# Kernel tuning notes

Measured on AMD Instinct MI355X. Metric: run time of the kernel, lower is better.

Reference implementation:

```python
import jax, jax.numpy as jnp
import numpy as np

B, S, D = 32, 8192, 128
SPARSITY = 0.5
CLUSTER = 4
HID = 256
MEM = 128
NCLS = 10
MASK_KEY = jax.random.key(1234)


def setup_inputs() -> dict:
    key = jax.random.key(0)
    ks = jax.random.split(key, 8)
    cin = CLUSTER * D  # 512
    return {
        "x": jax.random.normal(ks[0], (B, S, D), dtype=jnp.float32),
        "memory": jax.random.normal(ks[1], (B, MEM), dtype=jnp.float32),
        "W_fc": jax.random.normal(ks[2], (HID, cin), dtype=jnp.float32) / np.sqrt(cin),
        "b_fc": jax.random.normal(ks[3], (HID,), dtype=jnp.float32) * 0.01,
        "W_mem": jax.random.normal(ks[4], (MEM, HID), dtype=jnp.float32) / np.sqrt(HID),
        "b_mem": jax.random.normal(ks[5], (MEM,), dtype=jnp.float32) * 0.01,
        "W_out": jax.random.normal(ks[6], (NCLS, MEM), dtype=jnp.float32) / np.sqrt(MEM),
        "b_out": jax.random.normal(ks[7], (NCLS,), dtype=jnp.float32) * 0.01,
    }


def reference(x, memory, W_fc, b_fc, W_mem, b_mem, W_out, b_out):
    # --- SparseInformationExtraction: top-k tokens by L2 norm ---
    k = int(SPARSITY * S)  # 4096
    token_norms = jnp.linalg.norm(x, axis=-1)          # (B, S)
    _, topk_idx = jax.lax.top_k(token_norms, k)        # (B, k), sorted desc like torch.topk
    sparse_x = jnp.take_along_axis(x, topk_idx[:, :, None], axis=1)  # (B, k, D)

    # --- HierarchicalClustering: group CLUSTER tokens ---
    num_clusters = k // CLUSTER                        # 1024
    clustered = sparse_x.reshape(B, num_clusters, CLUSTER * D)  # (B, 1024, 512)

    # --- DynamicMaskingActivation: linear + bernoulli mask + relu ---
    h = jnp.einsum('bnc,hc->bnh', clustered, W_fc) + b_fc       # (B, 1024, HID)
    mask = jax.random.bernoulli(MASK_KEY, p=SPARSITY, shape=h.shape).astype(h.dtype)
    h = jax.nn.relu(h * mask)

    # --- SparseMemory: mean-pool + linear + residual relu ---
    x_compressed = jnp.mean(h, axis=1)                           # (B, HID)
    updated_memory = jax.nn.relu(x_compressed @ W_mem.T + b_mem + memory)  # (B, MEM)

    # --- output head ---
    output = updated_memory @ W_out.T + b_out                    # (B, NCLS)
    return (output, updated_memory)
```

## Files before the change

### kernel.cpp

```cpp
#include <hip/hip_runtime.h>
#include <stdint.h>

#define NB 32
#define NS 8192
#define ND 128
#define KTOP 4096
#define NCLUST 1024
#define CIN 512
#define HIDN 256
#define NMEM 128
#define NCLS 10
#define HALFCNT 4194304u

typedef unsigned long long ull;
typedef __attribute__((ext_vector_type(8))) short bf16x8;
typedef __attribute__((ext_vector_type(4))) float f32x4;

__device__ __forceinline__ unsigned int rotl32(unsigned int v, int r) {
  return (v << r) | (v >> (32 - r));
}

__device__ __forceinline__ void threefry_block(unsigned int& x0, unsigned int& x1) {
  const unsigned int k0 = 0u;
  const unsigned int k1 = 1234u;
  const unsigned int k2 = 0x1BD11BDAu ^ 0u ^ 1234u;
  x0 += k0; x1 += k1;
#define TF_R(r) { x0 += x1; x1 = rotl32(x1, (r)); x1 ^= x0; }
  TF_R(13) TF_R(15) TF_R(26) TF_R(6)   x0 += k1; x1 += k2 + 1u;
  TF_R(17) TF_R(29) TF_R(16) TF_R(24)  x0 += k2; x1 += k0 + 2u;
  TF_R(13) TF_R(15) TF_R(26) TF_R(6)   x0 += k0; x1 += k1 + 3u;
  TF_R(17) TF_R(29) TF_R(16) TF_R(24)  x0 += k1; x1 += k2 + 4u;
  TF_R(13) TF_R(15) TF_R(26) TF_R(6)   x0 += k2; x1 += k0 + 5u;
#undef TF_R
}

__device__ __forceinline__ bool mask_keep(unsigned int flat) {
  const bool low = flat < HALFCNT;
  unsigned int a, b;
  if (low) { a = flat;           b = flat + HALFCNT; }
  else     { a = flat - HALFCNT; b = flat; }
  threefry_block(a, b);
  const unsigned int w = low ? a : b;
  return (w & 0x80000000u) == 0u;
}

__device__ __forceinline__ unsigned int f2bf(float f) {
  unsigned int u = __float_as_uint(f);
  return (u + 0x7fffu + ((u >> 16) & 1u)) >> 16;
}
__device__ __forceinline__ unsigned int pack2bf(float lo, float hi) {
  return f2bf(lo) | (f2bf(hi) << 16);
}

__device__ __forceinline__ void gload_lds16(const void* g, void* l) {
  __builtin_amdgcn_global_load_lds(
      (const __attribute__((address_space(1))) unsigned int*)g,
      (__attribute__((address_space(3))) unsigned int*)l, 16, 0, 0);
}

__device__ __forceinline__ ull shfl_xor_u64(ull x, int m) {
  unsigned int lo = (unsigned int)x, hi = (unsigned int)(x >> 32);
  lo = (unsigned int)__shfl_xor((int)lo, m);
  hi = (unsigned int)__shfl_xor((int)hi, m);
  return ((ull)hi << 32) | lo;
}

__global__ __launch_bounds__(256) void wprep_kernel(
    const float* __restrict__ Wfc, unsigned short* __restrict__ Wbf) {
  const int t = blockIdx.x * 256 + threadIdx.x;
  const float4* s = (const float4*)(Wfc + (size_t)t * 8);
  const float4 a = s[0], b = s[1];
  uint4 o;
  o.x = pack2bf(a.x, a.y); o.y = pack2bf(a.z, a.w);
  o.z = pack2bf(b.x, b.y); o.w = pack2bf(b.z, b.w);
  *(uint4*)(Wbf + (size_t)t * 8) = o;
}

__global__ __launch_bounds__(256) void norms_kernel(
    const float* __restrict__ x, ull* __restrict__ keys,
    float* __restrict__ xc) {
  const int t = blockIdx.x * 256 + threadIdx.x;
  if (t < NB * HIDN) xc[t] = 0.0f;
  const int token = t >> 5;
  const int l = t & 31;
  const float4 v = ((const float4*)(x + (size_t)token * ND))[l];
  float ss = v.x * v.x + v.y * v.y + v.z * v.z + v.w * v.w;
#pragma unroll
  for (int off = 16; off >= 1; off >>= 1) ss += __shfl_xor(ss, off);
  if (l == 0) {
    const float nrm = sqrtf(ss);
    const unsigned int ub = ~__float_as_uint(nrm);
    keys[token] = ((ull)ub << 32) | (unsigned int)(token & (NS - 1));
  }
}

#define CMPEX(J)                                                        \
  {                                                                     \
    _Pragma("unroll") for (int r = 0; r < 8; ++r) {                     \
      if ((r & (J)) == 0) {                                             \
        const int i0 = (tid << 3) + r;                                  \
        const bool up2 = ((i0 & k) == 0);                               \
        const ull lo = v[r], hi = v[r | (J)];                           \
        const ull mn = lo < hi ? lo : hi;                               \
        const ull mx = lo < hi ? hi : lo;                               \
        v[r] = up2 ? mn : mx;                                           \
        v[r | (J)] = up2 ? mx : mn;                                     \
      }                                                                 \
    }                                                                   \
  }

__global__ __launch_bounds__(1024) void sort_kernel(
    const ull* __restrict__ keys, unsigned int* __restrict__ topk) {
  __shared__ ull slds[NS];
  const int b = blockIdx.x;
  const int tid = threadIdx.x;
  ull v[8];
  const ull* src = keys + (size_t)b * NS + tid * 8;
#pragma unroll
  for (int r = 0; r < 8; ++r) v[r] = src[r];

  for (int k = 2; k <= NS; k <<= 1) {
    for (int j = k >> 1; j >= 512; j >>= 1) {
      __syncthreads();
#pragma unroll
      for (int r = 0; r < 8; ++r) slds[r * 1024 + tid] = v[r];
      __syncthreads();
      const int ptid = tid ^ (j >> 3);
      const bool up2 = (((tid << 3) & k) == 0);
      const bool lower = (((tid << 3) & j) == 0);
      const bool keepmin = (up2 == lower);
#pragma unroll
      for (int r = 0; r < 8; ++r) {
        const ull p = slds[r * 1024 + ptid];
        const ull mn = v[r] < p ? v[r] : p;
        const ull mx = v[r] < p ? p : v[r];
        v[r] = keepmin ? mn : mx;
      }
    }
    {
      int jstart = (k >> 1) < 256 ? (k >> 1) : 256;
      for (int j = jstart; j >= 8; j >>= 1) {
        const int lanemask = j >> 3;
        const bool up2 = (((tid << 3) & k) == 0);
        const bool lower = (((tid << 3) & j) == 0);
        const bool keepmin = (up2 == lower);
#pragma unroll
        for (int r = 0; r < 8; ++r) {
          const ull p = shfl_xor_u64(v[r], lanemask);
          const ull mn = v[r] < p ? v[r] : p;
          const ull mx = v[r] < p ? p : v[r];
          v[r] = keepmin ? mn : mx;
        }
      }
    }
    if (k >= 8)      { CMPEX(4) CMPEX(2) CMPEX(1) }
    else if (k == 4) { CMPEX(2) CMPEX(1) }
    else             { CMPEX(1) }
  }

  if (tid < KTOP / 8) {
#pragma unroll
    for (int r = 0; r < 8; ++r)
      topk[b * KTOP + tid * 8 + r] = (unsigned int)v[r];
  }
}

__global__ __launch_bounds__(256) void gemm_kernel(
    const float* __restrict__ x, const unsigned short* __restrict__ Wbf,
    const float* __restrict__ bfc, const unsigned int* __restrict__ topk,
    float* __restrict__ xc) {
  __shared__ __align__(16) unsigned short Al[128 * 64];
  __shared__ __align__(16) unsigned short Bl[128 * 64];
  __shared__ int tokL[512];
  __shared__ float red[4][64];

  const int bid = blockIdx.x;
  const int m0 = bid * 128;
  const int bb = bid >> 3;
  const int n0 = blockIdx.y * 128;
  const int t = threadIdx.x;
  const int w = t >> 6, l = t & 63;
  const int wr = w >> 1, wc = w & 1;
  const int lrow = l & 15, lk = l >> 4;

  {
    const int base = bb * KTOP + (bid & 7) * 512;
    tokL[t] = (int)topk[base + t];
    tokL[t + 256] = (int)topk[base + t + 256];
  }
  __syncthreads();

  f32x4 acc[4][4];
#pragma unroll
  for (int m = 0; m < 4; ++m)
#pragma unroll
    for (int n = 0; n < 4; ++n) acc[m][n] = (f32x4)0.f;

  const int arow = t >> 1, kh = t & 1;
  float4 ar[8];
  {
    const int token = tokL[arow * 4 + 0];
    const float* asrc = x + ((size_t)bb * NS + token) * ND + kh * 32;
#pragma unroll
    for (int q = 0; q < 8; ++q) ar[q] = ((const float4*)asrc)[q];
  }

  const int brow_in8 = l >> 3;
  const int bkb_src = ((l & 7) * 16) ^ (brow_in8 << 4);

  for (int kt = 0; kt < 8; ++kt) {
    {
      const int kb0 = kh * 64;
#pragma unroll
      for (int c = 0; c < 4; ++c) {
        const float4 lo = ar[c * 2], hi = ar[c * 2 + 1];
        uint4 pw;
        pw.x = pack2bf(lo.x, lo.y); pw.y = pack2bf(lo.z, lo.w);
        pw.z = pack2bf(hi.x, hi.y); pw.w = pack2bf(hi.z, hi.w);
        const int kb = kb0 + c * 16;
        const int off = arow * 128 + (kb ^ ((arow & 7) << 4));
        *(uint4*)((char*)Al + off) = pw;
      }
    }
    {
#pragma unroll
      for (int q = 0; q < 4; ++q) {
        const int grp = w * 4 + q;
        const int row = grp * 8 + brow_in8;
        const char* g = (const char*)Wbf + (size_t)(n0 + row) * 1024 +
                        kt * 128 + bkb_src;
        gload_lds16(g, (char*)Bl + grp * 1024);
      }
    }
    __syncthreads();

    if (kt < 7) {
      const int c = kt + 1;
      const int token = tokL[arow * 4 + (c >> 1)];
      const float* asrc =
          x + ((size_t)bb * NS + token) * ND + (c & 1) * 64 + kh * 32;
#pragma unroll
      for (int q = 0; q < 8; ++q) ar[q] = ((const float4*)asrc)[q];
    }

    const int swz = (lrow & 7) << 4;
#pragma unroll
    for (int kk = 0; kk < 2; ++kk) {
      const int koff = (kk * 64 + lk * 16) ^ swz;
      bf16x8 af[4], bfr[4];
#pragma unroll
      for (int m = 0; m < 4; ++m)
        af[m] = *(const bf16x8*)((const char*)Al +
                                 (wr * 64 + m * 16 + lrow) * 128 + koff);
#pragma unroll
      for (int n = 0; n < 4; ++n)
        bfr[n] = *(const bf16x8*)((const char*)Bl +
                                  (wc * 64 + n * 16 + lrow) * 128 + koff);
#pragma unroll
      for (int m = 0; m < 4; ++m)
#pragma unroll
        for (int n = 0; n < 4; ++n)
          acc[m][n] = __builtin_amdgcn_mfma_f32_16x16x32_bf16(
              af[m], bfr[n], acc[m][n], 0, 0, 0);
    }
    __syncthreads();
  }

  float bias_n[4];
#pragma unroll
  for (int n = 0; n < 4; ++n) bias_n[n] = bfc[n0 + wc * 64 + n * 16 + lrow];

  const int rowbase = m0 + wr * 64 + lk * 4;
  float csum[4] = {0.f, 0.f, 0.f, 0.f};
#pragma unroll
  for (int n = 0; n < 4; ++n) {
    const unsigned int gcol = (unsigned int)(n0 + wc * 64 + n * 16 + lrow);
#pragma unroll
    for (int m = 0; m < 4; ++m) {
#pragma unroll
      for (int reg = 0; reg < 4; ++reg) {
        const unsigned int gm = (unsigned int)(rowbase + m * 16 + reg);
        const unsigned int flat = gm * 256u + gcol;
        const bool keep = mask_keep(flat);
        float vv = acc[m][n][reg] + bias_n[n];
        vv = keep ? fmaxf(vv, 0.0f) : 0.0f;
        csum[n] += vv;
      }
    }
  }
#pragma unroll
  for (int n = 0; n < 4; ++n) {
    csum[n] += __shfl_xor(csum[n], 16);
    csum[n] += __shfl_xor(csum[n], 32);
  }
  if (l < 16) {
#pragma unroll
    for (int n = 0; n < 4; ++n) red[w][n * 16 + l] = csum[n];
  }
  __syncthreads();
  if (t < 128) {
    const int cwc = t >> 6, c = t & 63;
    const float s = red[cwc][c] + red[cwc + 2][c];
    atomicAdd(&xc[bb * HIDN + n0 + t], s);
  }
}

__global__ __launch_bounds__(128) void tail_kernel(
    const float* __restrict__ xc, const float* __restrict__ memory,
    const float* __restrict__ Wmem, const float* __restrict__ bmem,
    const float* __restrict__ Wout, const float* __restrict__ bout,
    float* __restrict__ out) {
  __shared__ __align__(16) float xl[HIDN];
  __shared__ float ul[NMEM];
  const int b = blockIdx.x, t = threadIdx.x;
  xl[t]       = xc[b * HIDN + t] * (1.0f / NCLUST);
  xl[t + 128] = xc[b * HIDN + t + 128] * (1.0f / NCLUST);
  __syncthreads();
  float a = 0.0f;
  const float4* wr2 = (const float4*)(Wmem + (size_t)t * HIDN);
#pragma unroll 4
  for (int q = 0; q < HIDN / 4; ++q) {
    const float4 wv = wr2[q];
    const float4 xv = *(const float4*)&xl[q * 4];
    a = fmaf(wv.x, xv.x, a); a = fmaf(wv.y, xv.y, a);
    a = fmaf(wv.z, xv.z, a); a = fmaf(wv.w, xv.w, a);
  }
  a += bmem[t] + memory[b * NMEM + t];
  a = fmaxf(a, 0.0f);
  ul[t] = a;
  out[NB * NCLS + b * NMEM + t] = a;
  __syncthreads();
  if (t < NCLS) {
    float o = 0.0f;
#pragma unroll 4
    for (int m = 0; m < NMEM; ++m) o = fmaf(ul[m], Wout[t * NMEM + m], o);
    out[b * NCLS + t] = o + bout[t];
  }
}

extern "C" void kernel_launch(void* const* d_in, const int* in_sizes, int n_in,
                              void* d_out, int out_size, void* d_ws, size_t ws_size,
                              hipStream_t stream) {
  (void)in_sizes; (void)n_in; (void)out_size; (void)ws_size;
  const float* x    = (const float*)d_in[0];
  const float* mem  = (const float*)d_in[1];
  const float* Wfc  = (const float*)d_in[2];
  const float* bfc  = (const float*)d_in[3];
  const float* Wmem = (const float*)d_in[4];
  const float* bmem = (const float*)d_in[5];
  const float* Wout = (const float*)d_in[6];
  const float* bout = (const float*)d_in[7];
  float* out = (float*)d_out;

  char* ws = (char*)d_ws;
  ull* keys = (ull*)ws;
  unsigned int* topk = (unsigned int*)(ws + (size_t)NB * NS * 8);
  float* xc = (float*)(ws + (size_t)NB * NS * 8 + (size_t)NB * KTOP * 4);
  unsigned short* Wbf = (unsigned short*)(ws + (size_t)NB * NS * 8 +
                                          (size_t)NB * KTOP * 4 +
                                          (size_t)NB * HIDN * 4);

  wprep_kernel<<<dim3(HIDN * CIN / (256 * 8)), 256, 0, stream>>>(Wfc, Wbf);
  norms_kernel<<<dim3(NB * NS / 8), 256, 0, stream>>>(x, keys, xc);
  sort_kernel<<<dim3(NB), 1024, 0, stream>>>(keys, topk);
  gemm_kernel<<<dim3(256, 2), 256, 0, stream>>>(x, Wbf, bfc, topk, xc);
  tail_kernel<<<dim3(NB), 128, 0, stream>>>(xc, mem, Wmem, bmem, Wout, bout, out);
}
```

Measured before the change: 305.5 us.

## Split bitonic sort across two blocks per batch, widen GEMM tile, fuse weight prep

The per-batch 8192-key bitonic sort is split in two. A first kernel sorts each 4096-key half in opposite directions on 64 blocks. A second kernel takes the elementwise min of the two halves, which gives a bitonic sequence holding the top 4096, and runs only the final half-merge. The GEMM now covers all 256 hidden columns per 512-thread block, so each gathered x row is loaded once instead of twice. The weight bf16 conversion is folded into extra blocks of the norms kernel to save a launch. The cost is more sort launches and a bigger LDS footprint in the GEMM.

```diff
diff --git a/kernel.cpp b/kernel.cpp
--- a/kernel.cpp
+++ b/kernel.cpp
@@ -65,21 +65,23 @@
   return ((ull)hi << 32) | lo;
 }
 
-__global__ __launch_bounds__(256) void wprep_kernel(
-    const float* __restrict__ Wfc, unsigned short* __restrict__ Wbf) {
-  const int t = blockIdx.x * 256 + threadIdx.x;
-  const float4* s = (const float4*)(Wfc + (size_t)t * 8);
-  const float4 a = s[0], b = s[1];
-  uint4 o;
-  o.x = pack2bf(a.x, a.y); o.y = pack2bf(a.z, a.w);
-  o.z = pack2bf(b.x, b.y); o.w = pack2bf(b.z, b.w);
-  *(uint4*)(Wbf + (size_t)t * 8) = o;
-}
-
+#define NORM_BLOCKS 32768
 __global__ __launch_bounds__(256) void norms_kernel(
     const float* __restrict__ x, ull* __restrict__ keys,
-    float* __restrict__ xc) {
-  const int t = blockIdx.x * 256 + threadIdx.x;
+    float* __restrict__ xc, const float* __restrict__ Wfc,
+    unsigned short* __restrict__ Wbf) {
+  const int blk = blockIdx.x;
+  if (blk >= NORM_BLOCKS) {
+    const int t = (blk - NORM_BLOCKS) * 256 + threadIdx.x;
+    const float4* s = (const float4*)(Wfc + (size_t)t * 8);
+    const float4 a = s[0], b = s[1];
+    uint4 o;
+    o.x = pack2bf(a.x, a.y); o.y = pack2bf(a.z, a.w);
+    o.z = pack2bf(b.x, b.y); o.w = pack2bf(b.z, b.w);
+    *(uint4*)(Wbf + (size_t)t * 8) = o;
+    return;
+  }
+  const int t = blk * 256 + threadIdx.x;
   if (t < NB * HIDN) xc[t] = 0.0f;
   const int token = t >> 5;
   const int l = t & 31;
@@ -94,12 +96,12 @@
   }
 }
 
-#define CMPEX(J)                                                        \
+#define CMPEX(J, K, HF)                                                 \
   {                                                                     \
     _Pragma("unroll") for (int r = 0; r < 8; ++r) {                     \
       if ((r & (J)) == 0) {                                             \
         const int i0 = (tid << 3) + r;                                  \
-        const bool up2 = ((i0 & k) == 0);                               \
+        const bool up2 = (((i0 & (K)) == 0) != (HF));                   \
         const ull lo = v[r], hi = v[r | (J)];                           \
         const ull mn = lo < hi ? lo : hi;                               \
         const ull mx = lo < hi ? hi : lo;                               \
@@ -109,39 +111,40 @@
     }                                                                   \
   }
 
-__global__ __launch_bounds__(1024) void sort_kernel(
-    const ull* __restrict__ keys, unsigned int* __restrict__ topk) {
-  __shared__ ull slds[NS];
-  const int b = blockIdx.x;
+__global__ __launch_bounds__(512) void sortA_kernel(ull* __restrict__ keys) {
+  __shared__ ull slds[8 * 512];
+  const int b = blockIdx.x >> 1;
+  const int half = blockIdx.x & 1;
+  const bool hf = (half != 0);
   const int tid = threadIdx.x;
   ull v[8];
-  const ull* src = keys + (size_t)b * NS + tid * 8;
-#pragma unroll
-  for (int r = 0; r < 8; ++r) v[r] = src[r];
-
-  for (int k = 2; k <= NS; k <<= 1) {
+  ull* base = keys + (size_t)b * NS + half * 4096;
+#pragma unroll
+  for (int r = 0; r < 8; ++r) v[r] = base[tid * 8 + r];
+
+  for (int k = 2; k <= 4096; k <<= 1) {
     for (int j = k >> 1; j >= 512; j >>= 1) {
       __syncthreads();
 #pragma unroll
-      for (int r = 0; r < 8; ++r) slds[r * 1024 + tid] = v[r];
+      for (int r = 0; r < 8; ++r) slds[r * 512 + tid] = v[r];
       __syncthreads();
       const int ptid = tid ^ (j >> 3);
-      const bool up2 = (((tid << 3) & k) == 0);
+      const bool up2 = ((((tid << 3) & k) == 0) != hf);
       const bool lower = (((tid << 3) & j) == 0);
       const bool keepmin = (up2 == lower);
 #pragma unroll
       for (int r = 0; r < 8; ++r) {
-        const ull p = slds[r * 1024 + ptid];
+        const ull p = slds[r * 512 + ptid];
         const ull mn = v[r] < p ? v[r] : p;
         const ull mx = v[r] < p ? p : v[r];
         v[r] = keepmin ? mn : mx;
       }
     }
     {
-      int jstart = (k >> 1) < 256 ? (k >> 1) : 256;
+      const int jstart = (k >> 1) < 256 ? (k >> 1) : 256;
       for (int j = jstart; j >= 8; j >>= 1) {
         const int lanemask = j >> 3;
-        const bool up2 = (((tid << 3) & k) == 0);
+        const bool up2 = ((((tid << 3) & k) == 0) != hf);
         const bool lower = (((tid << 3) & j) == 0);
         const bool keepmin = (up2 == lower);
 #pragma unroll
@@ -153,56 +156,95 @@
         }
       }
     }
-    if (k >= 8)      { CMPEX(4) CMPEX(2) CMPEX(1) }
-    else if (k == 4) { CMPEX(2) CMPEX(1) }
-    else             { CMPEX(1) }
-  }
-
-  if (tid < KTOP / 8) {
-#pragma unroll
-    for (int r = 0; r < 8; ++r)
-      topk[b * KTOP + tid * 8 + r] = (unsigned int)v[r];
-  }
-}
-
-__global__ __launch_bounds__(256) void gemm_kernel(
+    if (k >= 8)      { CMPEX(4, k, hf) CMPEX(2, k, hf) CMPEX(1, k, hf) }
+    else if (k == 4) { CMPEX(2, k, hf) CMPEX(1, k, hf) }
+    else             { CMPEX(1, k, hf) }
+  }
+
+#pragma unroll
+  for (int r = 0; r < 8; ++r) base[tid * 8 + r] = v[r];
+}
+
+__global__ __launch_bounds__(512) void sortB_kernel(
+    const ull* __restrict__ keys, unsigned int* __restrict__ topk) {
+  __shared__ ull slds[8 * 512];
+  const int b = blockIdx.x;
+  const int tid = threadIdx.x;
+  ull v[8];
+  const ull* base = keys + (size_t)b * NS;
+#pragma unroll
+  for (int r = 0; r < 8; ++r) v[r] = base[tid * 8 + r];
+#pragma unroll
+  for (int r = 0; r < 8; ++r) {
+    const ull u = base[4096 + tid * 8 + r];
+    v[r] = v[r] < u ? v[r] : u;
+  }
+  for (int j = 2048; j >= 512; j >>= 1) {
+    __syncthreads();
+#pragma unroll
+    for (int r = 0; r < 8; ++r) slds[r * 512 + tid] = v[r];
+    __syncthreads();
+    const int ptid = tid ^ (j >> 3);
+    const bool keepmin = (((tid << 3) & j) == 0);
+#pragma unroll
+    for (int r = 0; r < 8; ++r) {
+      const ull p = slds[r * 512 + ptid];
+      const ull mn = v[r] < p ? v[r] : p;
+      const ull mx = v[r] < p ? p : v[r];
+      v[r] = keepmin ? mn : mx;
+    }
+  }
+  for (int j = 256; j >= 8; j >>= 1) {
+    const int lanemask = j >> 3;
+    const bool keepmin = (((tid << 3) & j) == 0);
+#pragma unroll
+    for (int r = 0; r < 8; ++r) {
+      const ull p = shfl_xor_u64(v[r], lanemask);
+      const ull mn = v[r] < p ? v[r] : p;
+      const ull mx = v[r] < p ? p : v[r];
+      v[r] = keepmin ? mn : mx;
+    }
+  }
+  CMPEX(4, 8192, false) CMPEX(2, 8192, false) CMPEX(1, 8192, false)
+#pragma unroll
+  for (int r = 0; r < 8; ++r)
+    topk[b * KTOP + tid * 8 + r] = (unsigned int)v[r];
+}
+
+__global__ __launch_bounds__(512) void gemm_kernel(
     const float* __restrict__ x, const unsigned short* __restrict__ Wbf,
     const float* __restrict__ bfc, const unsigned int* __restrict__ topk,
     float* __restrict__ xc) {
   __shared__ __align__(16) unsigned short Al[128 * 64];
-  __shared__ __align__(16) unsigned short Bl[128 * 64];
+  __shared__ __align__(16) unsigned short Bl[256 * 64];
   __shared__ int tokL[512];
-  __shared__ float red[4][64];
+  __shared__ float red[8][64];
 
   const int bid = blockIdx.x;
-  const int m0 = bid * 128;
   const int bb = bid >> 3;
-  const int n0 = blockIdx.y * 128;
+  const int m0 = (bid & 7) * 128;
   const int t = threadIdx.x;
   const int w = t >> 6, l = t & 63;
-  const int wr = w >> 1, wc = w & 1;
+  const int wr = w >> 2, wc = w & 3;
   const int lrow = l & 15, lk = l >> 4;
 
+  tokL[t] = (int)topk[bb * KTOP + m0 * 4 + t];
+  __syncthreads();
+
+  f32x4 acc[4][4];
+#pragma unroll
+  for (int m = 0; m < 4; ++m)
+#pragma unroll
+    for (int n = 0; n < 4; ++n) acc[m][n] = (f32x4)0.f;
+
+  const int arow = t >> 2, aseg = t & 3;
+  float4 ar[4];
   {
-    const int base = bb * KTOP + (bid & 7) * 512;
-    tokL[t] = (int)topk[base + t];
-    tokL[t + 256] = (int)topk[base + t + 256];
-  }
-  __syncthreads();
-
-  f32x4 acc[4][4];
-#pragma unroll
-  for (int m = 0; m < 4; ++m)
-#pragma unroll
-    for (int n = 0; n < 4; ++n) acc[m][n] = (f32x4)0.f;
-
-  const int arow = t >> 1, kh = t & 1;
-  float4 ar[8];
-  {
-    const int token = tokL[arow * 4 + 0];
-    const float* asrc = x + ((size_t)bb * NS + token) * ND + kh * 32;
-#pragma unroll
-    for (int q = 0; q < 8; ++q) ar[q] = ((const float4*)asrc)[q];
+    const int cs = aseg;
+    const int token = tokL[arow * 4 + (cs >> 3)];
+    const float* asrc = x + ((size_t)bb * NS + token) * ND + ((cs * 16) & 127);
+#pragma unroll
+    for (int q = 0; q < 4; ++q) ar[q] = ((const float4*)asrc)[q];
   }
 
   const int brow_in8 = l >> 3;
@@ -210,37 +252,34 @@
 
   for (int kt = 0; kt < 8; ++kt) {
     {
-      const int kb0 = kh * 64;
-#pragma unroll
-      for (int c = 0; c < 4; ++c) {
-        const float4 lo = ar[c * 2], hi = ar[c * 2 + 1];
-        uint4 pw;
-        pw.x = pack2bf(lo.x, lo.y); pw.y = pack2bf(lo.z, lo.w);
-        pw.z = pack2bf(hi.x, hi.y); pw.w = pack2bf(hi.z, hi.w);
-        const int kb = kb0 + c * 16;
-        const int off = arow * 128 + (kb ^ ((arow & 7) << 4));
-        *(uint4*)((char*)Al + off) = pw;
-      }
+      uint4 p0, p1;
+      p0.x = pack2bf(ar[0].x, ar[0].y); p0.y = pack2bf(ar[0].z, ar[0].w);
+      p0.z = pack2bf(ar[1].x, ar[1].y); p0.w = pack2bf(ar[1].z, ar[1].w);
+      p1.x = pack2bf(ar[2].x, ar[2].y); p1.y = pack2bf(ar[2].z, ar[2].w);
+      p1.z = pack2bf(ar[3].x, ar[3].y); p1.w = pack2bf(ar[3].z, ar[3].w);
+      const int swz = (arow & 7) << 4;
+      const int base = arow * 128;
+      *(uint4*)((char*)Al + base + ((aseg * 32) ^ swz)) = p0;
+      *(uint4*)((char*)Al + base + ((aseg * 32 + 16) ^ swz)) = p1;
     }
     {
 #pragma unroll
       for (int q = 0; q < 4; ++q) {
-        const int grp = w * 4 + q;
+        const int grp = q * 8 + w;
         const int row = grp * 8 + brow_in8;
-        const char* g = (const char*)Wbf + (size_t)(n0 + row) * 1024 +
-                        kt * 128 + bkb_src;
+        const char* g = (const char*)Wbf + (size_t)row * 1024 + kt * 128 +
+                        bkb_src;
         gload_lds16(g, (char*)Bl + grp * 1024);
       }
     }
     __syncthreads();
 
     if (kt < 7) {
-      const int c = kt + 1;
-      const int token = tokL[arow * 4 + (c >> 1)];
-      const float* asrc =
-          x + ((size_t)bb * NS + token) * ND + (c & 1) * 64 + kh * 32;
-#pragma unroll
-      for (int q = 0; q < 8; ++q) ar[q] = ((const float4*)asrc)[q];
+      const int cs = (kt + 1) * 4 + aseg;
+      const int token = tokL[arow * 4 + (cs >> 3)];
+      const float* asrc = x + ((size_t)bb * NS + token) * ND + ((cs * 16) & 127);
+#pragma unroll
+      for (int q = 0; q < 4; ++q) ar[q] = ((const float4*)asrc)[q];
     }
 
     const int swz = (lrow & 7) << 4;
@@ -268,18 +307,19 @@
 
   float bias_n[4];
 #pragma unroll
-  for (int n = 0; n < 4; ++n) bias_n[n] = bfc[n0 + wc * 64 + n * 16 + lrow];
+  for (int n = 0; n < 4; ++n) bias_n[n] = bfc[wc * 64 + n * 16 + lrow];
 
   const int rowbase = m0 + wr * 64 + lk * 4;
   float csum[4] = {0.f, 0.f, 0.f, 0.f};
 #pragma unroll
   for (int n = 0; n < 4; ++n) {
-    const unsigned int gcol = (unsigned int)(n0 + wc * 64 + n * 16 + lrow);
+    const unsigned int gcol = (unsigned int)(wc * 64 + n * 16 + lrow);
 #pragma unroll
     for (int m = 0; m < 4; ++m) {
 #pragma unroll
       for (int reg = 0; reg < 4; ++reg) {
-        const unsigned int gm = (unsigned int)(rowbase + m * 16 + reg);
+        const unsigned int gm =
+            (unsigned int)(bb * NCLUST + rowbase + m * 16 + reg);
         const unsigned int flat = gm * 256u + gcol;
         const bool keep = mask_keep(flat);
         float vv = acc[m][n][reg] + bias_n[n];
@@ -298,10 +338,10 @@
     for (int n = 0; n < 4; ++n) red[w][n * 16 + l] = csum[n];
   }
   __syncthreads();
-  if (t < 128) {
+  if (t < HIDN) {
     const int cwc = t >> 6, c = t & 63;
-    const float s = red[cwc][c] + red[cwc + 2][c];
-    atomicAdd(&xc[bb * HIDN + n0 + t], s);
+    const float s = red[cwc][c] + red[cwc + 4][c];
+    atomicAdd(&xc[bb * HIDN + t], s);
   }
 }
 
@@ -360,9 +400,10 @@
                                           (size_t)NB * KTOP * 4 +
                                           (size_t)NB * HIDN * 4);
 
-  wprep_kernel<<<dim3(HIDN * CIN / (256 * 8)), 256, 0, stream>>>(Wfc, Wbf);
-  norms_kernel<<<dim3(NB * NS / 8), 256, 0, stream>>>(x, keys, xc);
-  sort_kernel<<<dim3(NB), 1024, 0, stream>>>(keys, topk);
-  gemm_kernel<<<dim3(256, 2), 256, 0, stream>>>(x, Wbf, bfc, topk, xc);
+  norms_kernel<<<dim3(NORM_BLOCKS + 64), 256, 0, stream>>>(x, keys, xc, Wfc,
+                                                           Wbf);
+  sortA_kernel<<<dim3(NB * 2), 512, 0, stream>>>(keys);
+  sortB_kernel<<<dim3(NB), 512, 0, stream>>>(keys, topk);
+  gemm_kernel<<<dim3(256), 512, 0, stream>>>(x, Wbf, bfc, topk, xc);
   tail_kernel<<<dim3(NB), 128, 0, stream>>>(xc, mem, Wmem, bmem, Wout, bout, out);
 }
```

Measured after the change: 277.0 us. 9.3% less time.
